# Kernel tuning notes

Measured on AMD Instinct MI355X. Metric: run time of the kernel, lower is better.

Reference implementation:

```python
import jax, jax.numpy as jnp
import numpy as np

B, T = 32, 4096
QD, MD, AD = 1024, 512, 128
F, K = 32, 31
PAD = (K - 1) // 2  # 'same' padding as in Tacotron-2 location conv


def setup_inputs() -> dict:
    key = jax.random.key(0)
    ks = jax.random.split(key, 12)
    s = lambda fan_in: 1.0 / np.sqrt(fan_in)
    return {
        "query": jax.random.normal(ks[0], (B, QD), jnp.float32),
        "memory": jax.random.normal(ks[1], (B, T, MD), jnp.float32),
        "alignments": jax.random.uniform(ks[2], (B, T, 2), jnp.float32),
        "mask": jnp.zeros((B, T), dtype=bool),
        "Wq": jax.random.normal(ks[3], (QD, AD), jnp.float32) * s(QD),
        "bq": jnp.zeros((AD,), jnp.float32),
        "Wm": jax.random.normal(ks[4], (MD, AD), jnp.float32) * s(MD),
        "bm": jnp.zeros((AD,), jnp.float32),
        "conv_w": jax.random.normal(ks[5], (F, 2, K), jnp.float32) * s(2 * K),
        "conv_b": jnp.zeros((F,), jnp.float32),
        "Wl": jax.random.normal(ks[6], (F, AD), jnp.float32) * s(F),
        "bl": jnp.zeros((AD,), jnp.float32),
        "v_w": jax.random.normal(ks[7], (AD,), jnp.float32) * s(AD),
        "v_b": jnp.zeros((), jnp.float32),
    }


def reference(query, memory, alignments, mask, Wq, bq, Wm, bm, conv_w, conv_b, Wl, bl, v_w, v_b):
    # processed memory: [B, T, AD]
    processed_memory = jnp.einsum("btm,ma->bta", memory, Wm) + bm
    # processed query: [B, 1, AD] (query.unsqueeze(1))
    processed_query = (query @ Wq + bq)[:, None, :]
    # location features: conv over time on [B, 2, T] -> [B, F, T]
    a = jnp.transpose(alignments, (0, 2, 1))  # [B, 2, T]
    loc = jax.lax.conv_general_dilated(
        a, conv_w, window_strides=(1,), padding=[(PAD, PAD)],
        dimension_numbers=("NCH", "OIH", "NCH"))
    loc = loc + conv_b[None, :, None]
    loc = jnp.transpose(loc, (0, 2, 1))  # [B, T, F]
    processed_loc = jnp.einsum("btf,fa->bta", loc, Wl) + bl
    # additive score: v . tanh(q + m + l)  -> [B, T]
    score = jnp.einsum("bta,a->bt", jnp.tanh(processed_query + processed_memory + processed_loc), v_w) + v_b
    score = jnp.where(mask, -jnp.inf, score)
    alignment = jax.nn.softmax(score, axis=-1)  # [B, T]
    context = jnp.einsum("bt,btm->bm", alignment, memory)  # [B, MD]
    return context, alignment
```

## Files before the change

kernel.cpp:

```cpp
#include <hip/hip_runtime.h>
#include <math.h>

#define B_ 32
#define T_ 4096
#define QD_ 1024
#define MD_ 512
#define AD_ 128
#define F_ 32
#define K_ 31
#define PAD_ 15

#define TT 32
#define NBLK (T_ / TT)

typedef float f32x16 __attribute__((ext_vector_type(16)));
typedef unsigned int uint4v __attribute__((ext_vector_type(4)));

__device__ inline unsigned pk_bf2(float lo, float hi) {
    unsigned ul = __float_as_uint(lo) + 0x8000u;
    unsigned uh = __float_as_uint(hi) + 0x8000u;
    return __builtin_amdgcn_perm(uh, ul, 0x07060302u);
}

__device__ inline unsigned short f2bf_rn(float f) {
    unsigned u = __float_as_uint(f);
    u += 0x7fffu + ((u >> 16) & 1u);
    return (unsigned short)(u >> 16);
}

__device__ inline float bf2f(unsigned short u) {
    return __uint_as_float(((unsigned)u) << 16);
}

__device__ inline void mfma32(f32x16& c, uint4v a, uint4v b) {
    asm("s_nop 1\n\tv_mfma_f32_32x32x16_bf16 %0, %1, %2, %0"
        : "+v"(c) : "v"(a), "v"(b));
}

__global__ __launch_bounds__(256) void k_prep(const float* __restrict__ Wm,
                                              unsigned short* __restrict__ wmT_sw) {
    int gid = blockIdx.x * 256 + threadIdx.x;
    int kk = gid >> 8;
    int ct = (gid >> 6) & 3;
    int lane = gid & 63;
    int k0 = kk * 16 + (lane >> 5) * 8;
    int a = ct * 32 + (lane & 31);
    unsigned short o[8];
#pragma unroll
    for (int j = 0; j < 8; j++) o[j] = f2bf_rn(Wm[(k0 + j) * AD_ + a]);
    uint4v v;
    v[0] = ((unsigned)o[1] << 16) | o[0];
    v[1] = ((unsigned)o[3] << 16) | o[2];
    v[2] = ((unsigned)o[5] << 16) | o[4];
    v[3] = ((unsigned)o[7] << 16) | o[6];
    *(uint4v*)(wmT_sw + (long)gid * 8) = v;
}

__global__ __launch_bounds__(128) void k_pq(const float* __restrict__ query,
                                            const float* __restrict__ Wq,
                                            float* __restrict__ pq) {
    int b = blockIdx.x;
    int qc = blockIdx.y;
    int a = threadIdx.x;
    const float* qrow = query + b * QD_ + qc * 128;
    const float* wq = Wq + (qc * 128) * AD_ + a;
    float acc = 0.f;
#pragma unroll 4
    for (int i = 0; i < 128; i++) acc += qrow[i] * wq[i * AD_];
    atomicAdd(&pq[b * AD_ + a], acc);
}

__global__ __launch_bounds__(256) void k_ploc(
    const float* __restrict__ alignments, const float* __restrict__ convw,
    const float* __restrict__ convb, const float* __restrict__ Wl,
    const float* __restrict__ bl, const float* __restrict__ bm,
    const float* __restrict__ bq, const float* __restrict__ pq,
    unsigned short* __restrict__ ploc) {
    __shared__ float s_cw[F_ * 2 * K_];
    __shared__ float s_al[(128 + K_ - 1) * 2];
    __shared__ float s_loc[128 * F_];

    const int tid = threadIdx.x;
    const int b = blockIdx.y;
    const int t0 = blockIdx.x * 128;

    for (int i = tid; i < F_ * 2 * K_; i += 256) s_cw[i] = convw[i];
    for (int i = tid; i < (128 + K_ - 1) * 2; i += 256) {
        int tg = t0 + (i >> 1) - PAD_;
        s_al[i] = (tg >= 0 && tg < T_) ? alignments[((long)b * T_ + tg) * 2 + (i & 1)] : 0.f;
    }
    __syncthreads();

    for (int i = tid; i < 128 * F_; i += 256) {
        int f = i & (F_ - 1);
        int t = i >> 5;
        float acc = convb[f];
        const float* w0 = &s_cw[f * (2 * K_)];
        const float* w1 = w0 + K_;
        const float2* ap = (const float2*)&s_al[t * 2];
#pragma unroll
        for (int k = 0; k < K_; k++) {
            float2 a2 = ap[k];
            acc += a2.x * w0[k] + a2.y * w1[k];
        }
        s_loc[t * F_ + f] = acc;
    }
    __syncthreads();

    const int a = tid & 127;
    float wl[F_];
#pragma unroll
    for (int f = 0; f < F_; f++) wl[f] = Wl[f * AD_ + a];
    const float base = pq[b * AD_ + a] + bq[a] + bm[a] + bl[a];
    unsigned short* outp = ploc + ((long)b * T_ + t0) * AD_ + a;
    for (int t = (tid >> 7); t < 128; t += 2) {
        float acc = base;
        const float* lr = &s_loc[t * F_];
#pragma unroll
        for (int f = 0; f < F_; f++) acc += lr[f] * wl[f];
        outp[(long)t * AD_] = f2bf_rn(acc);
    }
}

__global__ __launch_bounds__(64) void k_score_ctx(
    const float* __restrict__ memory, const unsigned char* __restrict__ mask,
    const unsigned short* __restrict__ wmT_sw, const unsigned short* __restrict__ ploc,
    const float* __restrict__ vw, const float* __restrict__ vb,
    float* __restrict__ bmax, float* __restrict__ bden,
    float* __restrict__ num, float* __restrict__ oalign) {
    __shared__ __align__(16) float s_sc[TT];
    __shared__ __align__(16) float s_w[TT];

    const int lane = threadIdx.x;
    const int l31 = lane & 31;
    const int h = lane >> 5;
    const int b = blockIdx.y;
    const int blk = blockIdx.x;
    const int t0 = blk * TT;

    const float* aptr = memory + ((long)b * T_ + t0) * MD_;
    const float* arow = aptr + l31 * MD_ + h * 8;
    const unsigned short* bpk = wmT_sw + lane * 8;

    f32x16 c0, c1, c2, c3;
#pragma unroll
    for (int i = 0; i < 16; i++) { c0[i] = 0.f; c1[i] = 0.f; c2[i] = 0.f; c3[i] = 0.f; }

    for (int cc = 0; cc < 16; ++cc) {
        const float4 p0 = *(const float4*)(arow + cc * 32);
        const float4 p1 = *(const float4*)(arow + cc * 32 + 4);
        const float4 p2 = *(const float4*)(arow + cc * 32 + 16);
        const float4 p3 = *(const float4*)(arow + cc * 32 + 20);
        const int kb0 = (2 * cc) * 2048;
        const int kb1 = kb0 + 2048;
        uint4v b00 = *(const uint4v*)(bpk + kb0);
        uint4v b01 = *(const uint4v*)(bpk + kb0 + 512);
        uint4v b02 = *(const uint4v*)(bpk + kb0 + 1024);
        uint4v b03 = *(const uint4v*)(bpk + kb0 + 1536);
        uint4v b10 = *(const uint4v*)(bpk + kb1);
        uint4v b11 = *(const uint4v*)(bpk + kb1 + 512);
        uint4v b12 = *(const uint4v*)(bpk + kb1 + 1024);
        uint4v b13 = *(const uint4v*)(bpk + kb1 + 1536);
        uint4v af0, af1;
        af0[0] = pk_bf2(p0.x, p0.y); af0[1] = pk_bf2(p0.z, p0.w);
        af0[2] = pk_bf2(p1.x, p1.y); af0[3] = pk_bf2(p1.z, p1.w);
        af1[0] = pk_bf2(p2.x, p2.y); af1[1] = pk_bf2(p2.z, p2.w);
        af1[2] = pk_bf2(p3.x, p3.y); af1[3] = pk_bf2(p3.z, p3.w);
        mfma32(c0, af0, b00); mfma32(c1, af0, b01);
        mfma32(c2, af0, b02); mfma32(c3, af0, b03);
        mfma32(c0, af1, b10); mfma32(c1, af1, b11);
        mfma32(c2, af1, b12); mfma32(c3, af1, b13);
    }
    asm volatile("s_nop 7\n\ts_nop 7\n\ts_nop 7" ::: "memory");

    const unsigned short* plp = ploc + ((long)b * T_ + t0) * AD_ + l31;
    const float vw0 = vw[l31];
    const float vw1 = vw[32 + l31];
    const float vw2 = vw[64 + l31];
    const float vw3 = vw[96 + l31];
#pragma unroll
    for (int i = 0; i < 16; i++) {
        const int row = (i & 3) + 8 * (i >> 2) + 4 * h;
        const unsigned short* pr = plp + row * AD_;
        float s = tanhf(c0[i] + bf2f(pr[0]))  * vw0
                + tanhf(c1[i] + bf2f(pr[32])) * vw1
                + tanhf(c2[i] + bf2f(pr[64])) * vw2
                + tanhf(c3[i] + bf2f(pr[96])) * vw3;
        s += __shfl_xor(s, 1);
        s += __shfl_xor(s, 2);
        s += __shfl_xor(s, 4);
        s += __shfl_xor(s, 8);
        s += __shfl_xor(s, 16);
        if (l31 == 0) s_sc[row] = s;
    }

    if (lane < TT) {
        float s = s_sc[lane] + vb[0];
        if (mask[(long)b * T_ + t0 + lane]) s = -INFINITY;
        s_sc[lane] = s;
    }
    float m = -INFINITY;
#pragma unroll
    for (int r = 0; r < TT; r++) m = fmaxf(m, s_sc[r]);
    float e = 0.f;
    if (lane < TT) {
        e = (m == -INFINITY) ? 0.f : expf(s_sc[lane] - m);
        s_w[lane] = e;
        oalign[(long)b * T_ + t0 + lane] = e;
    }
    float d = e;
    d += __shfl_xor(d, 1);
    d += __shfl_xor(d, 2);
    d += __shfl_xor(d, 4);
    d += __shfl_xor(d, 8);
    d += __shfl_xor(d, 16);
    if (lane == 0) { bmax[b * NBLK + blk] = m; bden[b * NBLK + blk] = d; }

    const float2* mp = (const float2*)aptr + lane;
    float2 a0 = make_float2(0.f, 0.f), a1 = make_float2(0.f, 0.f);
    float2 a2 = make_float2(0.f, 0.f), a3 = make_float2(0.f, 0.f);
#pragma unroll 8
    for (int t = 0; t < TT; t++) {
        const float wt = s_w[t];
        const float2 v0 = mp[t * 256];
        const float2 v1 = mp[t * 256 + 64];
        const float2 v2 = mp[t * 256 + 128];
        const float2 v3 = mp[t * 256 + 192];
        a0.x += wt * v0.x; a0.y += wt * v0.y;
        a1.x += wt * v1.x; a1.y += wt * v1.y;
        a2.x += wt * v2.x; a2.y += wt * v2.y;
        a3.x += wt * v3.x; a3.y += wt * v3.y;
    }
    float2* np = (float2*)(num + ((long)b * NBLK + blk) * MD_) + lane;
    np[0] = a0; np[64] = a1; np[128] = a2; np[192] = a3;
}

__global__ __launch_bounds__(512) void k_reduce(
    const float* __restrict__ bmax, const float* __restrict__ bden,
    const float* __restrict__ num,
    float* __restrict__ ctx, float* __restrict__ oalign) {
    int b = blockIdx.x;
    int tid = threadIdx.x;
    __shared__ float sm[NBLK], sf[NBLK];
    __shared__ float sD;
    if (tid < NBLK) sm[tid] = bmax[b * NBLK + tid];
    __syncthreads();
    float M = -INFINITY;
#pragma unroll 8
    for (int i = 0; i < NBLK; i++) M = fmaxf(M, sm[i]);
    if (tid < NBLK) sf[tid] = expf(sm[tid] - M);
    __syncthreads();
    if (tid == 0) {
        float D = 0.f;
        for (int i = 0; i < NBLK; i++) D += sf[i] * bden[b * NBLK + i];
        sD = D;
    }
    __syncthreads();
    const float invD = 1.f / sD;

    float acc = 0.f;
    const float* np = num + (long)b * NBLK * MD_ + tid;
#pragma unroll 8
    for (int blk = 0; blk < NBLK; blk++) acc += sf[blk] * np[blk * MD_];
    ctx[b * MD_ + tid] = acc * invD;

    for (int t = tid; t < T_; t += 512) {
        oalign[(long)b * T_ + t] *= sf[t >> 5] * invD;
    }
}

extern "C" void kernel_launch(void* const* d_in, const int* in_sizes, int n_in,
                              void* d_out, int out_size, void* d_ws, size_t ws_size,
                              hipStream_t stream) {
    const float* query      = (const float*)d_in[0];
    const float* memory     = (const float*)d_in[1];
    const float* alignments = (const float*)d_in[2];
    const unsigned char* mask = (const unsigned char*)d_in[3];
    const float* Wq    = (const float*)d_in[4];
    const float* bq    = (const float*)d_in[5];
    const float* Wm    = (const float*)d_in[6];
    const float* bm    = (const float*)d_in[7];
    const float* convw = (const float*)d_in[8];
    const float* convb = (const float*)d_in[9];
    const float* Wl    = (const float*)d_in[10];
    const float* bl    = (const float*)d_in[11];
    const float* vw    = (const float*)d_in[12];
    const float* vb    = (const float*)d_in[13];

    float* out = (float*)d_out;
    float* ctx = out;
    float* oalign = out + B_ * MD_;

    float* ws = (float*)d_ws;
    float* pq     = ws;
    float* bmax   = pq + B_ * AD_;
    float* bden   = bmax + B_ * NBLK;
    float* num    = bden + B_ * NBLK;
    unsigned short* wmT_sw = (unsigned short*)(num + (long)B_ * NBLK * MD_);
    unsigned short* ploc   = wmT_sw + (long)8192 * 8;

    hipMemsetAsync(pq, 0, B_ * AD_ * sizeof(float), stream);

    k_prep<<<32, 256, 0, stream>>>(Wm, wmT_sw);
    k_pq<<<dim3(B_, QD_ / 128), 128, 0, stream>>>(query, Wq, pq);
    k_ploc<<<dim3(T_ / 128, B_), 256, 0, stream>>>(alignments, convw, convb, Wl, bl, bm, bq, pq, ploc);
    k_score_ctx<<<dim3(NBLK, B_), 64, 0, stream>>>(
        memory, mask, wmT_sw, ploc, vw, vb, bmax, bden, num, oalign);
    k_reduce<<<B_, 512, 0, stream>>>(bmax, bden, num, ctx, oalign);
}
```

Before: 557.8 us.

## Stage memory tiles via async global-to-LDS loads and fuse softmax reduction into score kernel

The score kernel now processes 128 timesteps per 256-thread block, streaming memory tiles into double-buffered, XOR-swizzled LDS through global_load_lds so the next tile loads while MFMAs run on the current one. The final cross-block softmax and context reduction moves into the last-arriving block via an atomic counter, which removes the separate reduce kernel. The Wm prep and query projection are merged into one launch, and the query projection writes per-chunk partials instead of using atomics and a memset. The exchange is a per-iteration block barrier, more LDS use, and fewer, larger blocks.

```diff
diff --git a/kernel.cpp b/kernel.cpp
--- a/kernel.cpp
+++ b/kernel.cpp
@@ -10,7 +10,7 @@
 #define K_ 31
 #define PAD_ 15
 
-#define TT 32
+#define TT 128
 #define NBLK (T_ / TT)
 
 typedef float f32x16 __attribute__((ext_vector_type(16)));
@@ -37,44 +37,56 @@
         : "+v"(c) : "v"(a), "v"(b));
 }
 
-__global__ __launch_bounds__(256) void k_prep(const float* __restrict__ Wm,
-                                              unsigned short* __restrict__ wmT_sw) {
-    int gid = blockIdx.x * 256 + threadIdx.x;
-    int kk = gid >> 8;
-    int ct = (gid >> 6) & 3;
-    int lane = gid & 63;
-    int k0 = kk * 16 + (lane >> 5) * 8;
-    int a = ct * 32 + (lane & 31);
-    unsigned short o[8];
-#pragma unroll
-    for (int j = 0; j < 8; j++) o[j] = f2bf_rn(Wm[(k0 + j) * AD_ + a]);
-    uint4v v;
-    v[0] = ((unsigned)o[1] << 16) | o[0];
-    v[1] = ((unsigned)o[3] << 16) | o[2];
-    v[2] = ((unsigned)o[5] << 16) | o[4];
-    v[3] = ((unsigned)o[7] << 16) | o[6];
-    *(uint4v*)(wmT_sw + (long)gid * 8) = v;
-}
-
-__global__ __launch_bounds__(128) void k_pq(const float* __restrict__ query,
-                                            const float* __restrict__ Wq,
-                                            float* __restrict__ pq) {
-    int b = blockIdx.x;
-    int qc = blockIdx.y;
-    int a = threadIdx.x;
-    const float* qrow = query + b * QD_ + qc * 128;
-    const float* wq = Wq + (qc * 128) * AD_ + a;
+__device__ inline void gload_lds16(const float* g, void* lds) {
+    __builtin_amdgcn_global_load_lds(
+        (const __attribute__((address_space(1))) void*)g,
+        (__attribute__((address_space(3))) void*)lds, 16, 0, 0);
+}
+
+__global__ __launch_bounds__(256) void k_pre(
+    const float* __restrict__ Wm, unsigned short* __restrict__ wmT_sw,
+    const float* __restrict__ query, const float* __restrict__ Wq,
+    float* __restrict__ pqp, int* __restrict__ cnt) {
+    __shared__ float s_t[128];
+    const int bx = blockIdx.x;
+    const int tid = threadIdx.x;
+    if (bx < 32) {
+        int gid = bx * 256 + tid;
+        int kk = gid >> 8;
+        int ct = (gid >> 6) & 3;
+        int lane = gid & 63;
+        int k0 = kk * 16 + (lane >> 5) * 8;
+        int a = ct * 32 + (lane & 31);
+        unsigned short o[8];
+#pragma unroll
+        for (int j = 0; j < 8; j++) o[j] = f2bf_rn(Wm[(k0 + j) * AD_ + a]);
+        uint4v v;
+        v[0] = ((unsigned)o[1] << 16) | o[0];
+        v[1] = ((unsigned)o[3] << 16) | o[2];
+        v[2] = ((unsigned)o[5] << 16) | o[4];
+        v[3] = ((unsigned)o[7] << 16) | o[6];
+        *(uint4v*)(wmT_sw + (long)gid * 8) = v;
+        if (bx == 0 && tid < B_) cnt[tid] = 0;
+        return;
+    }
+    const int pb = bx - 32;
+    const int b = pb >> 3, qc = pb & 7;
+    const int a = tid & 127, hf = tid >> 7;
+    const float* qrow = query + b * QD_ + qc * 128 + hf * 64;
+    const float* wq = Wq + (qc * 128 + hf * 64) * AD_ + a;
     float acc = 0.f;
 #pragma unroll 4
-    for (int i = 0; i < 128; i++) acc += qrow[i] * wq[i * AD_];
-    atomicAdd(&pq[b * AD_ + a], acc);
+    for (int i = 0; i < 64; i++) acc += qrow[i] * wq[i * AD_];
+    if (hf) s_t[a] = acc;
+    __syncthreads();
+    if (!hf) pqp[((long)qc * B_ + b) * AD_ + a] = acc + s_t[a];
 }
 
 __global__ __launch_bounds__(256) void k_ploc(
     const float* __restrict__ alignments, const float* __restrict__ convw,
     const float* __restrict__ convb, const float* __restrict__ Wl,
     const float* __restrict__ bl, const float* __restrict__ bm,
-    const float* __restrict__ bq, const float* __restrict__ pq,
+    const float* __restrict__ bq, const float* __restrict__ pqp,
     unsigned short* __restrict__ ploc) {
     __shared__ float s_cw[F_ * 2 * K_];
     __shared__ float s_al[(128 + K_ - 1) * 2];
@@ -111,7 +123,10 @@
     float wl[F_];
 #pragma unroll
     for (int f = 0; f < F_; f++) wl[f] = Wl[f * AD_ + a];
-    const float base = pq[b * AD_ + a] + bq[a] + bm[a] + bl[a];
+    float pqv = 0.f;
+#pragma unroll
+    for (int q = 0; q < 8; q++) pqv += pqp[((long)q * B_ + b) * AD_ + a];
+    const float base = pqv + bq[a] + bm[a] + bl[a];
     unsigned short* outp = ploc + ((long)b * T_ + t0) * AD_ + a;
     for (int t = (tid >> 7); t < 128; t += 2) {
         float acc = base;
@@ -122,16 +137,24 @@
     }
 }
 
-__global__ __launch_bounds__(64) void k_score_ctx(
+__global__ __launch_bounds__(256) void k_score_ctx(
     const float* __restrict__ memory, const unsigned char* __restrict__ mask,
     const unsigned short* __restrict__ wmT_sw, const unsigned short* __restrict__ ploc,
     const float* __restrict__ vw, const float* __restrict__ vb,
     float* __restrict__ bmax, float* __restrict__ bden,
-    float* __restrict__ num, float* __restrict__ oalign) {
-    __shared__ __align__(16) float s_sc[TT];
-    __shared__ __align__(16) float s_w[TT];
-
-    const int lane = threadIdx.x;
+    float* __restrict__ num, float* __restrict__ oalign,
+    float* __restrict__ ctx, int* __restrict__ cnt) {
+    __shared__ __align__(16) float sA[2][128 * 32];
+    __shared__ float s_sc[TT];
+    __shared__ float s_w[TT];
+    __shared__ float s_red[8];
+    __shared__ float f_m[NBLK], f_f[NBLK];
+    __shared__ float f_Ds;
+    __shared__ int s_last;
+
+    const int tid = threadIdx.x;
+    const int w = tid >> 6;
+    const int lane = tid & 63;
     const int l31 = lane & 31;
     const int h = lane >> 5;
     const int b = blockIdx.y;
@@ -139,49 +162,77 @@
     const int t0 = blk * TT;
 
     const float* aptr = memory + ((long)b * T_ + t0) * MD_;
-    const float* arow = aptr + l31 * MD_ + h * 8;
+
+    const int srow = lane >> 3;
+    const int sc16 = (lane & 7) ^ srow;
+    const float* gA[4];
+#pragma unroll
+    for (int j = 0; j < 4; j++)
+        gA[j] = aptr + (long)((j * 4 + w) * 8 + srow) * MD_ + sc16 * 4;
+
+    const int Rl = w * 32 + l31;
+    const int rx = Rl & 7;
+    const int o_a0 = (Rl * 8 + ((2 * h) ^ rx)) * 16;
+    const int o_a1 = (Rl * 8 + ((2 * h + 1) ^ rx)) * 16;
+    const int o_b0 = (Rl * 8 + ((4 + 2 * h) ^ rx)) * 16;
+    const int o_b1 = (Rl * 8 + ((5 + 2 * h) ^ rx)) * 16;
+
     const unsigned short* bpk = wmT_sw + lane * 8;
 
     f32x16 c0, c1, c2, c3;
 #pragma unroll
     for (int i = 0; i < 16; i++) { c0[i] = 0.f; c1[i] = 0.f; c2[i] = 0.f; c3[i] = 0.f; }
 
-    for (int cc = 0; cc < 16; ++cc) {
-        const float4 p0 = *(const float4*)(arow + cc * 32);
-        const float4 p1 = *(const float4*)(arow + cc * 32 + 4);
-        const float4 p2 = *(const float4*)(arow + cc * 32 + 16);
-        const float4 p3 = *(const float4*)(arow + cc * 32 + 20);
-        const int kb0 = (2 * cc) * 2048;
-        const int kb1 = kb0 + 2048;
-        uint4v b00 = *(const uint4v*)(bpk + kb0);
-        uint4v b01 = *(const uint4v*)(bpk + kb0 + 512);
-        uint4v b02 = *(const uint4v*)(bpk + kb0 + 1024);
-        uint4v b03 = *(const uint4v*)(bpk + kb0 + 1536);
-        uint4v b10 = *(const uint4v*)(bpk + kb1);
-        uint4v b11 = *(const uint4v*)(bpk + kb1 + 512);
-        uint4v b12 = *(const uint4v*)(bpk + kb1 + 1024);
-        uint4v b13 = *(const uint4v*)(bpk + kb1 + 1536);
+#pragma unroll
+    for (int j = 0; j < 4; j++)
+        gload_lds16(gA[j], (char*)(&sA[0][0]) + (j * 4 + w) * 1024);
+    __syncthreads();
+
+#pragma unroll 2
+    for (int c = 0; c < 16; ++c) {
+        const int cb = c & 1;
+        if (c < 15) {
+#pragma unroll
+            for (int j = 0; j < 4; j++)
+                gload_lds16(gA[j] + (c + 1) * 32,
+                            (char*)(&sA[cb ^ 1][0]) + (j * 4 + w) * 1024);
+        }
+        const unsigned short* bc = bpk + (c << 12);
+        uint4v b00 = *(const uint4v*)(bc);
+        uint4v b01 = *(const uint4v*)(bc + 512);
+        uint4v b02 = *(const uint4v*)(bc + 1024);
+        uint4v b03 = *(const uint4v*)(bc + 1536);
+        uint4v b10 = *(const uint4v*)(bc + 2048);
+        uint4v b11 = *(const uint4v*)(bc + 2560);
+        uint4v b12 = *(const uint4v*)(bc + 3072);
+        uint4v b13 = *(const uint4v*)(bc + 3584);
+        const char* ab = (const char*)(&sA[cb][0]);
+        float4 q0 = *(const float4*)(ab + o_a0);
+        float4 q1 = *(const float4*)(ab + o_a1);
+        float4 q2 = *(const float4*)(ab + o_b0);
+        float4 q3 = *(const float4*)(ab + o_b1);
         uint4v af0, af1;
-        af0[0] = pk_bf2(p0.x, p0.y); af0[1] = pk_bf2(p0.z, p0.w);
-        af0[2] = pk_bf2(p1.x, p1.y); af0[3] = pk_bf2(p1.z, p1.w);
-        af1[0] = pk_bf2(p2.x, p2.y); af1[1] = pk_bf2(p2.z, p2.w);
-        af1[2] = pk_bf2(p3.x, p3.y); af1[3] = pk_bf2(p3.z, p3.w);
+        af0[0] = pk_bf2(q0.x, q0.y); af0[1] = pk_bf2(q0.z, q0.w);
+        af0[2] = pk_bf2(q1.x, q1.y); af0[3] = pk_bf2(q1.z, q1.w);
+        af1[0] = pk_bf2(q2.x, q2.y); af1[1] = pk_bf2(q2.z, q2.w);
+        af1[2] = pk_bf2(q3.x, q3.y); af1[3] = pk_bf2(q3.z, q3.w);
         mfma32(c0, af0, b00); mfma32(c1, af0, b01);
         mfma32(c2, af0, b02); mfma32(c3, af0, b03);
         mfma32(c0, af1, b10); mfma32(c1, af1, b11);
         mfma32(c2, af1, b12); mfma32(c3, af1, b13);
+        __syncthreads();
     }
     asm volatile("s_nop 7\n\ts_nop 7\n\ts_nop 7" ::: "memory");
 
-    const unsigned short* plp = ploc + ((long)b * T_ + t0) * AD_ + l31;
+    const unsigned short* plp = ploc + ((long)b * T_ + t0 + w * 32) * AD_ + l31;
     const float vw0 = vw[l31];
     const float vw1 = vw[32 + l31];
     const float vw2 = vw[64 + l31];
     const float vw3 = vw[96 + l31];
 #pragma unroll
     for (int i = 0; i < 16; i++) {
-        const int row = (i & 3) + 8 * (i >> 2) + 4 * h;
-        const unsigned short* pr = plp + row * AD_;
+        const int crow = (i & 3) + 8 * (i >> 2) + 4 * h;
+        const unsigned short* pr = plp + crow * AD_;
         float s = tanhf(c0[i] + bf2f(pr[0]))  * vw0
                 + tanhf(c1[i] + bf2f(pr[32])) * vw1
                 + tanhf(c2[i] + bf2f(pr[64])) * vw2
@@ -191,22 +242,26 @@
         s += __shfl_xor(s, 4);
         s += __shfl_xor(s, 8);
         s += __shfl_xor(s, 16);
-        if (l31 == 0) s_sc[row] = s;
-    }
-
-    if (lane < TT) {
-        float s = s_sc[lane] + vb[0];
-        if (mask[(long)b * T_ + t0 + lane]) s = -INFINITY;
-        s_sc[lane] = s;
-    }
-    float m = -INFINITY;
-#pragma unroll
-    for (int r = 0; r < TT; r++) m = fmaxf(m, s_sc[r]);
+        if (l31 == 0) s_sc[w * 32 + crow] = s;
+    }
+    __syncthreads();
+
+    float sv = -INFINITY;
+    if (tid < TT) {
+        sv = s_sc[tid] + vb[0];
+        if (mask[(long)b * T_ + t0 + tid]) sv = -INFINITY;
+    }
+    float m = sv;
+#pragma unroll
+    for (int off = 32; off >= 1; off >>= 1) m = fmaxf(m, __shfl_xor(m, off));
+    if (lane == 0) s_red[w] = m;
+    __syncthreads();
+    m = fmaxf(fmaxf(s_red[0], s_red[1]), fmaxf(s_red[2], s_red[3]));
     float e = 0.f;
-    if (lane < TT) {
-        e = (m == -INFINITY) ? 0.f : expf(s_sc[lane] - m);
-        s_w[lane] = e;
-        oalign[(long)b * T_ + t0 + lane] = e;
+    if (tid < TT) {
+        e = (sv == -INFINITY) ? 0.f : expf(sv - m);
+        s_w[tid] = e;
+        oalign[(long)b * T_ + t0 + tid] = e;
     }
     float d = e;
     d += __shfl_xor(d, 1);
@@ -214,59 +269,61 @@
     d += __shfl_xor(d, 4);
     d += __shfl_xor(d, 8);
     d += __shfl_xor(d, 16);
-    if (lane == 0) { bmax[b * NBLK + blk] = m; bden[b * NBLK + blk] = d; }
-
-    const float2* mp = (const float2*)aptr + lane;
-    float2 a0 = make_float2(0.f, 0.f), a1 = make_float2(0.f, 0.f);
-    float2 a2 = make_float2(0.f, 0.f), a3 = make_float2(0.f, 0.f);
+    d += __shfl_xor(d, 32);
+    if (lane == 0) s_red[4 + w] = d;
+    __syncthreads();
+    if (tid == 0) {
+        bmax[b * NBLK + blk] = m;
+        bden[b * NBLK + blk] = s_red[4] + s_red[5] + s_red[6] + s_red[7];
+    }
+
+    {
+        const float2* mp = (const float2*)aptr + tid;
+        float ax = 0.f, ay = 0.f;
 #pragma unroll 8
-    for (int t = 0; t < TT; t++) {
-        const float wt = s_w[t];
-        const float2 v0 = mp[t * 256];
-        const float2 v1 = mp[t * 256 + 64];
-        const float2 v2 = mp[t * 256 + 128];
-        const float2 v3 = mp[t * 256 + 192];
-        a0.x += wt * v0.x; a0.y += wt * v0.y;
-        a1.x += wt * v1.x; a1.y += wt * v1.y;
-        a2.x += wt * v2.x; a2.y += wt * v2.y;
-        a3.x += wt * v3.x; a3.y += wt * v3.y;
-    }
-    float2* np = (float2*)(num + ((long)b * NBLK + blk) * MD_) + lane;
-    np[0] = a0; np[64] = a1; np[128] = a2; np[192] = a3;
-}
-
-__global__ __launch_bounds__(512) void k_reduce(
-    const float* __restrict__ bmax, const float* __restrict__ bden,
-    const float* __restrict__ num,
-    float* __restrict__ ctx, float* __restrict__ oalign) {
-    int b = blockIdx.x;
-    int tid = threadIdx.x;
-    __shared__ float sm[NBLK], sf[NBLK];
-    __shared__ float sD;
-    if (tid < NBLK) sm[tid] = bmax[b * NBLK + tid];
+        for (int t = 0; t < TT; t++) {
+            const float2 v = mp[t * 256];
+            const float wt = s_w[t];
+            ax += wt * v.x;
+            ay += wt * v.y;
+        }
+        float2 o; o.x = ax; o.y = ay;
+        *(float2*)(num + ((long)b * NBLK + blk) * MD_ + tid * 2) = o;
+    }
+
+    __threadfence();
+    __syncthreads();
+    if (tid == 0) s_last = (atomicAdd(&cnt[b], 1) == NBLK - 1) ? 1 : 0;
+    __syncthreads();
+    if (!s_last) return;
+    __threadfence();
+
+    if (tid < NBLK) f_m[tid] = bmax[b * NBLK + tid];
     __syncthreads();
     float M = -INFINITY;
-#pragma unroll 8
-    for (int i = 0; i < NBLK; i++) M = fmaxf(M, sm[i]);
-    if (tid < NBLK) sf[tid] = expf(sm[tid] - M);
+#pragma unroll
+    for (int i = 0; i < NBLK; i++) M = fmaxf(M, f_m[i]);
+    if (tid < NBLK) f_f[tid] = (f_m[tid] == -INFINITY) ? 0.f : expf(f_m[tid] - M);
     __syncthreads();
     if (tid == 0) {
         float D = 0.f;
-        for (int i = 0; i < NBLK; i++) D += sf[i] * bden[b * NBLK + i];
-        sD = D;
-    }
-    __syncthreads();
-    const float invD = 1.f / sD;
-
-    float acc = 0.f;
-    const float* np = num + (long)b * NBLK * MD_ + tid;
+        for (int i = 0; i < NBLK; i++) D += f_f[i] * bden[b * NBLK + i];
+        f_Ds = D;
+    }
+    __syncthreads();
+    const float invD = 1.f / f_Ds;
+
+#pragma unroll
+    for (int g = 0; g < 2; g++) {
+        const int col = tid + g * 256;
+        float acc = 0.f;
 #pragma unroll 8
-    for (int blk = 0; blk < NBLK; blk++) acc += sf[blk] * np[blk * MD_];
-    ctx[b * MD_ + tid] = acc * invD;
-
-    for (int t = tid; t < T_; t += 512) {
-        oalign[(long)b * T_ + t] *= sf[t >> 5] * invD;
-    }
+        for (int k2 = 0; k2 < NBLK; k2++)
+            acc += f_f[k2] * num[((long)b * NBLK + k2) * MD_ + col];
+        ctx[b * MD_ + col] = acc * invD;
+    }
+    for (int t = tid; t < T_; t += 256)
+        oalign[(long)b * T_ + t] *= f_f[t >> 7] * invD;
 }
 
 extern "C" void kernel_launch(void* const* d_in, const int* in_sizes, int n_in,
@@ -292,19 +349,16 @@
     float* oalign = out + B_ * MD_;
 
     float* ws = (float*)d_ws;
-    float* pq     = ws;
-    float* bmax   = pq + B_ * AD_;
-    float* bden   = bmax + B_ * NBLK;
-    float* num    = bden + B_ * NBLK;
-    unsigned short* wmT_sw = (unsigned short*)(num + (long)B_ * NBLK * MD_);
-    unsigned short* ploc   = wmT_sw + (long)8192 * 8;
-
-    hipMemsetAsync(pq, 0, B_ * AD_ * sizeof(float), stream);
-
-    k_prep<<<32, 256, 0, stream>>>(Wm, wmT_sw);
-    k_pq<<<dim3(B_, QD_ / 128), 128, 0, stream>>>(query, Wq, pq);
-    k_ploc<<<dim3(T_ / 128, B_), 256, 0, stream>>>(alignments, convw, convb, Wl, bl, bm, bq, pq, ploc);
-    k_score_ctx<<<dim3(NBLK, B_), 64, 0, stream>>>(
-        memory, mask, wmT_sw, ploc, vw, vb, bmax, bden, num, oalign);
-    k_reduce<<<B_, 512, 0, stream>>>(bmax, bden, num, ctx, oalign);
-}
+    float* pqp  = ws;
+    float* bmax = pqp + 8 * B_ * AD_;
+    float* bden = bmax + B_ * NBLK;
+    float* num  = bden + B_ * NBLK;
+    int* cnt    = (int*)(num + (long)B_ * NBLK * MD_);
+    unsigned short* wmT_sw = (unsigned short*)(cnt + B_);
+    unsigned short* ploc   = wmT_sw + (long)65536;
+
+    k_pre<<<288, 256, 0, stream>>>(Wm, wmT_sw, query, Wq, pqp, cnt);
+    k_ploc<<<dim3(T_ / 128, B_), 256, 0, stream>>>(alignments, convw, convb, Wl, bl, bm, bq, pqp, ploc);
+    k_score_ctx<<<dim3(NBLK, B_), 256, 0, stream>>>(
+        memory, mask, wmT_sw, ploc, vw, vb, bmax, bden, num, oalign, ctx, cnt);
+}
```

Measured after the change: 727.3 us. +30.4%, slower.
